# Kernel tuning notes

Hardware: AMD Instinct MI355X
Metric: run time of the kernel (lower is better)

## Reference

```python
import jax, jax.numpy as jnp
import numpy as np

B, C, H, W = 8, 4, 96, 96
HW = H * W
PCT = 95.0            # TRUNCATED_HAUSDORFF_PERCENTILE
IGNORE = 0            # HD_IGNORE_CLASS_INDEX


def setup_inputs() -> dict:
    key = jax.random.key(0)
    k1, k2 = jax.random.split(key)
    predictions = jax.random.normal(k1, (B, C, H, W), dtype=jnp.float32)
    labels = jax.random.randint(k2, (B, H, W), 0, C, dtype=jnp.int32)
    return {"predictions": predictions, "labels": labels}


def _masked_percentile(vals, mask, q):
    """np.percentile(vals[mask], q) with linear interpolation; invalid -> +inf sort to end."""
    n = jnp.sum(mask)
    s = jnp.sort(jnp.where(mask, vals, jnp.inf))
    pos = (q / 100.0) * jnp.maximum(n - 1, 0).astype(vals.dtype)
    lo = jnp.floor(pos).astype(jnp.int32)
    hi = jnp.ceil(pos).astype(jnp.int32)
    frac = pos - lo.astype(vals.dtype)
    return s[lo] * (1.0 - frac) + s[hi] * frac


def _hausdorff(predictions, labels):
    # argmax of softmax == argmax of logits, but keep the softmax for faithfulness
    pred_cls = jnp.argmax(jax.nn.softmax(predictions, axis=1), axis=1)  # [B,H,W]
    cls_ids = jnp.arange(C)
    mask_a = (pred_cls[:, None] == cls_ids[None, :, None, None]).reshape(B * C, HW)  # pred one-hot
    mask_b = (labels[:, None] == cls_ids[None, :, None, None]).reshape(B * C, HW)    # label one-hot

    # Pixel coordinates (row, col) as in np.argwhere; pairwise Euclidean distances once.
    ys, xs = jnp.meshgrid(jnp.arange(H), jnp.arange(W), indexing="ij")
    coords = jnp.stack([ys.ravel(), xs.ravel()], axis=1).astype(jnp.float32)  # [HW,2]
    sq = jnp.sum(coords * coords, axis=1)
    D = jnp.sqrt(jnp.maximum(sq[:, None] + sq[None, :] - 2.0 * (coords @ coords.T), 0.0))  # [HW,HW]

    def per_pair(masks):
        ma, mb = masks  # [HW] bool each
        fwd_min = jnp.min(jnp.where(mb[None, :], D, jnp.inf), axis=1)  # min dist A-pixel -> B set
        rev_min = jnp.min(jnp.where(ma[:, None], D, jnp.inf), axis=0)  # min dist B-pixel -> A set
        f = _masked_percentile(fwd_min, ma, PCT)
        r = _masked_percentile(rev_min, mb, PCT)
        return jnp.stack([f, r, jnp.maximum(f, r)])

    res = jax.lax.map(per_pair, (mask_a, mask_b)).reshape(B, C, 3)
    valid = (jnp.arange(C) != IGNORE)
    per_class = jnp.where(valid[None, :, None], res, 0.0).mean(axis=0)  # [C,3] mean over batch

    def finalize(v):  # v: [C] -> [C+2]: per-class, mean(all), mean(excluding class 0)
        return jnp.concatenate([v, jnp.mean(v)[None], jnp.mean(v[1:])[None]])

    FHD = finalize(per_class[:, 0])
    RHD = finalize(per_class[:, 1])
    MHD = finalize(per_class[:, 2])
    return MHD, FHD, RHD


def reference(predictions, labels):
    return _hausdorff(predictions, labels)
```

## Files before the change

kernel.cpp:

```cpp
#include <hip/hip_runtime.h>
#include <math.h>

#define B_   8
#define C_   4
#define H_   96
#define W_   96
#define HW_  9216
#define NBINS 18052
#define NH32 ((NBINS + 1) / 2)
#define NT   1024
#define NBLK 64
#define NW   16
#define NGRP 1152

__global__ __launch_bounds__(NT) void hd_main(const float* __restrict__ preds,
                                              const int*   __restrict__ labels,
                                              float* __restrict__ frws)
{
    __shared__ unsigned char  qmb[NGRP];
    __shared__ unsigned char  tmb[NGRP];
    __shared__ unsigned short g2u[HW_];
    __shared__ unsigned int   h32[NH32];
    __shared__ int twv[NW], qwv[NW], zwv[NW], bwv[NW];

    const int id  = blockIdx.x;
    const int dir = id & 1;
    const int bc  = id >> 1;
    const int b   = bc >> 2;
    const int c   = bc & 3;
    const int tid = threadIdx.x;
    const int lane = tid & 63;
    const int wid  = tid >> 6;

    const float* Pb = preds  + (size_t)b * C_ * HW_;
    const int*   Lb = labels + (size_t)b * HW_;

    for (int i = tid; i < NH32; i += NT) h32[i] = 0u;

    {
        int myT = 0, myQ = 0, myN0 = 0;
        #pragma unroll
        for (int k = 0; k < 2; ++k) {
            const int g = k * NT + tid;
            if (g < NGRP) {
                const int bp = g * 8;
                const float4 a0 = *(const float4*)(Pb + bp);
                const float4 b0 = *(const float4*)(Pb + bp + 4);
                const float4 a1 = *(const float4*)(Pb + HW_ + bp);
                const float4 b1 = *(const float4*)(Pb + HW_ + bp + 4);
                const float4 a2 = *(const float4*)(Pb + 2 * HW_ + bp);
                const float4 b2 = *(const float4*)(Pb + 2 * HW_ + bp + 4);
                const float4 a3 = *(const float4*)(Pb + 3 * HW_ + bp);
                const float4 b3 = *(const float4*)(Pb + 3 * HW_ + bp + 4);
                const int4   l0 = *(const int4*)(Lb + bp);
                const int4   l1 = *(const int4*)(Lb + bp + 4);
                unsigned tb = 0, qb = 0;
                #define PX_(j, e0, e1, e2, e3, lj)                              \
                {   int bi = 0; float bv = (e0);                                \
                    if ((e1) > bv) { bv = (e1); bi = 1; }                       \
                    if ((e2) > bv) { bv = (e2); bi = 2; }                       \
                    if ((e3) > bv) { bv = (e3); bi = 3; }                       \
                    const bool pm = (bi == c);                                  \
                    const bool lm = ((lj) == c);                                \
                    const bool qm = dir ? lm : pm;                              \
                    const bool tm = dir ? pm : lm;                              \
                    tb |= (unsigned)tm << (j); qb |= (unsigned)qm << (j); }
                PX_(0, a0.x, a1.x, a2.x, a3.x, l0.x)
                PX_(1, a0.y, a1.y, a2.y, a3.y, l0.y)
                PX_(2, a0.z, a1.z, a2.z, a3.z, l0.z)
                PX_(3, a0.w, a1.w, a2.w, a3.w, l0.w)
                PX_(4, b0.x, b1.x, b2.x, b3.x, l1.x)
                PX_(5, b0.y, b1.y, b2.y, b3.y, l1.y)
                PX_(6, b0.z, b1.z, b2.z, b3.z, l1.z)
                PX_(7, b0.w, b1.w, b2.w, b3.w, l1.w)
                #undef PX_
                tmb[g] = (unsigned char)tb;
                qmb[g] = (unsigned char)qb;
                myT  += __popc(tb);
                myQ  += __popc(qb);
                myN0 += __popc(tb & qb);
            }
        }
        #pragma unroll
        for (int d = 32; d >= 1; d >>= 1) {
            myT  += __shfl_xor(myT,  d, 64);
            myQ  += __shfl_xor(myQ,  d, 64);
            myN0 += __shfl_xor(myN0, d, 64);
        }
        if (lane == 0) { twv[wid] = myT; qwv[wid] = myQ; zwv[wid] = myN0; }
    }
    __syncthreads();

    int nT = 0;
    #pragma unroll
    for (int w = 0; w < NW; ++w) nT += twv[w];
    const int tEmpty = (nT == 0);

    for (int k = 0; k < HW_ / NT; ++k) {
        const int p = k * NT + tid;
        const int y = p / W_;
        const int x = p - y * W_;
        const unsigned r0 = *(const unsigned*)(tmb + 12 * y);
        const unsigned r1 = *(const unsigned*)(tmb + 12 * y + 4);
        const unsigned r2 = *(const unsigned*)(tmb + 12 * y + 8);
        const unsigned long long A  = (unsigned long long)r0 |
                                      ((unsigned long long)r1 << 32);
        const unsigned long long Bw = r2;

        int dl = 1000, dr = 1000;
        if (x < 64) {
            const unsigned long long ml = A & ((2ull << x) - 1ull);
            if (ml) dl = x - (63 - __builtin_clzll(ml));
            const unsigned long long mr = A & ~((1ull << x) - 1ull);
            if (mr)      dr = __builtin_ctzll(mr) - x;
            else if (Bw) dr = 64 + __builtin_ctzll(Bw) - x;
        } else {
            const int xb = x - 64;
            const unsigned long long ml = Bw & ((2ull << xb) - 1ull);
            if (ml)     dl = x - (64 + 63 - __builtin_clzll(ml));
            else if (A) dl = x - (63 - __builtin_clzll(A));
            const unsigned long long mr = Bw & ~((1ull << xb) - 1ull);
            if (mr) dr = 64 + __builtin_ctzll(mr) - x;
        }
        const int g = min(dl, dr);
        g2u[p] = (g >= 96) ? (unsigned short)40000
                           : (unsigned short)(g * g);
    }
    __syncthreads();

    {
        int bmax = 0;
        if (!tEmpty) {
            for (int k = 0; k < HW_ / NT; ++k) {
                const int p = k * NT + tid;
                const int byi = p >> 3, bsh = p & 7;
                if (!((qmb[byi] >> bsh) & 1)) continue;
                if ((tmb[byi] >> bsh) & 1) continue;
                const int y = p / W_;
                const int x = p - y * W_;
                const int a0 = (int)g2u[p];
                const int a1 = (y >= 1)     ? (int)g2u[p - W_]     : 0x7FFF0000;
                const int a2 = (y + 1 < H_) ? (int)g2u[p + W_]     : 0x7FFF0000;
                const int a3 = (y >= 2)     ? (int)g2u[p - 2 * W_] : 0x7FFF0000;
                const int a4 = (y + 2 < H_) ? (int)g2u[p + 2 * W_] : 0x7FFF0000;
                int best = min(a0, min(min(a1 + 1, a2 + 1), min(a3 + 4, a4 + 4)));
                for (int off = 3; off < H_; ++off) {
                    const int o2 = off * off;
                    if (o2 >= best) break;
                    const int r1 = y - off;
                    const int r2 = y + off;
                    if (r1 >= 0) best = min(best, o2 + (int)g2u[r1 * W_ + x]);
                    if (r2 < H_) best = min(best, o2 + (int)g2u[r2 * W_ + x]);
                }
                bmax = max(bmax, best);
                atomicAdd(&h32[best >> 1], 1u << ((best & 1) << 4));
            }
        }
        #pragma unroll
        for (int d = 32; d >= 1; d >>= 1) bmax = max(bmax, __shfl_xor(bmax, d, 64));
        if (lane == 0) bwv[wid] = bmax;
    }
    __syncthreads();

    if (wid != 0) return;

    int nQ = 0, n0s = 0, maxd2 = 0;
    #pragma unroll
    for (int w = 0; w < NW; ++w) {
        nQ += qwv[w]; n0s += zwv[w]; maxd2 = max(maxd2, bwv[w]);
    }
    const int h0x = tEmpty ? 0 : n0s;

    int nm1 = nQ - 1; if (nm1 < 0) nm1 = 0;
    const float posf = 0.95f * (float)nm1;
    const int lo = (int)floorf(posf);
    const int hi = (int)ceilf(posf);
    const float frac = posf - (float)lo;

    int svlo = -1, svhi = -1;
    if (!tEmpty) {
        int run = 0;
        for (int base = 0; base <= maxd2; base += 64) {
            const int i = base + lane;
            int h = 0;
            if (i <= maxd2) {
                h = (int)((h32[i >> 1] >> ((i & 1) << 4)) & 0xFFFFu);
                if (i == 0) h += h0x;
            }
            int inc = h;
            #pragma unroll
            for (int d = 1; d < 64; d <<= 1) {
                const int t = __shfl_up(inc, d, 64);
                if (lane >= d) inc += t;
            }
            const int excl = run + inc - h;
            if (h > 0) {
                if (excl <= lo && lo < excl + h) svlo = i;
                if (excl <= hi && hi < excl + h) svhi = i;
            }
            run += __shfl(inc, 63, 64);
        }
        #pragma unroll
        for (int d = 32; d >= 1; d >>= 1) {
            svlo = max(svlo, __shfl_xor(svlo, d, 64));
            svhi = max(svhi, __shfl_xor(svhi, d, 64));
        }
    }
    if (lane == 0) {
        const float vlo = (svlo < 0) ? __builtin_inff() : (float)sqrt((double)svlo);
        const float vhi = (svhi < 0) ? __builtin_inff() : (float)sqrt((double)svhi);
        frws[id] = vlo * (1.0f - frac) + vhi * frac;
    }
}

__global__ __launch_bounds__(64) void hd_fin(const float* __restrict__ frws,
                                             float* __restrict__ out)
{
    __shared__ float fr[NBLK];
    const int tid = threadIdx.x;
    fr[tid] = frws[tid];
    __syncthreads();
    if (tid == 0) {
        float F[4], R[4], M[4];
        for (int c = 0; c < 4; ++c) {
            if (c == 0) { F[c] = R[c] = M[c] = 0.0f; continue; }
            float sf = 0.0f, sr = 0.0f, sm = 0.0f;
            for (int b = 0; b < 8; ++b) {
                const float f = fr[((b * 4 + c) << 1) + 0];
                const float r = fr[((b * 4 + c) << 1) + 1];
                sf += f; sr += r;
                float m = f > r ? f : r;
                if (f != f || r != r) m = f + r;
                sm += m;
            }
            F[c] = sf / 8.0f; R[c] = sr / 8.0f; M[c] = sm / 8.0f;
        }
        float* o = out;
        o[0] = M[0]; o[1] = M[1]; o[2] = M[2]; o[3] = M[3];
        o[4] = (M[0] + M[1] + M[2] + M[3]) / 4.0f;
        o[5] = (M[1] + M[2] + M[3]) / 3.0f;
        o += 6;
        o[0] = F[0]; o[1] = F[1]; o[2] = F[2]; o[3] = F[3];
        o[4] = (F[0] + F[1] + F[2] + F[3]) / 4.0f;
        o[5] = (F[1] + F[2] + F[3]) / 3.0f;
        o += 6;
        o[0] = R[0]; o[1] = R[1]; o[2] = R[2]; o[3] = R[3];
        o[4] = (R[0] + R[1] + R[2] + R[3]) / 4.0f;
        o[5] = (R[1] + R[2] + R[3]) / 3.0f;
    }
}

extern "C" void kernel_launch(void* const* d_in, const int* in_sizes, int n_in,
                              void* d_out, int out_size, void* d_ws, size_t ws_size,
                              hipStream_t stream)
{
    const float* preds  = (const float*)d_in[0];
    const int*   labels = (const int*)d_in[1];
    float* frws = (float*)d_ws;

    hipLaunchKernelGGL(hd_main, dim3(NBLK), dim3(NT), 0, stream,
                       preds, labels, frws);
    hipLaunchKernelGGL(hd_fin, dim3(1), dim3(64), 0, stream,
                       frws, (float*)d_out);
}
```

Baseline: 20.40 us.

## Skip ignored class blocks, add per-warp low-bin histograms, parallelize finalize

The main grid shrinks from 64 to 48 blocks by never launching the class-0 blocks, since their result is zeroed anyway. Small squared distances below 128 now go into per-warp privatized shared histograms, which cuts atomic contention on hot bins. The prefix scan sums these per-warp copies for the low bins. The finalize kernel computes its 18 outputs in parallel across threads instead of on a single thread; the class-0 slots in the workspace are left unwritten but are not read.

```diff
diff --git a/kernel.cpp b/kernel.cpp
--- a/kernel.cpp
+++ b/kernel.cpp
@@ -9,9 +9,10 @@
 #define NBINS 18052
 #define NH32 ((NBINS + 1) / 2)
 #define NT   1024
-#define NBLK 64
 #define NW   16
 #define NGRP 1152
+#define NBLK 48
+#define HOT  128
 
 __global__ __launch_bounds__(NT) void hd_main(const float* __restrict__ preds,
                                               const int*   __restrict__ labels,
@@ -21,13 +22,15 @@
     __shared__ unsigned char  tmb[NGRP];
     __shared__ unsigned short g2u[HW_];
     __shared__ unsigned int   h32[NH32];
+    __shared__ unsigned int   whist[NW * (HOT / 2)];
     __shared__ int twv[NW], qwv[NW], zwv[NW], bwv[NW];
 
-    const int id  = blockIdx.x;
-    const int dir = id & 1;
-    const int bc  = id >> 1;
-    const int b   = bc >> 2;
-    const int c   = bc & 3;
+    const int bid = blockIdx.x;
+    const int b   = bid / 6;
+    const int rem = bid - b * 6;
+    const int c   = 1 + (rem >> 1);
+    const int dir = rem & 1;
+    const int id  = ((b * 4 + c) << 1) | dir;
     const int tid = threadIdx.x;
     const int lane = tid & 63;
     const int wid  = tid >> 6;
@@ -36,7 +39,7 @@
     const int*   Lb = labels + (size_t)b * HW_;
 
     for (int i = tid; i < NH32; i += NT) h32[i] = 0u;
-
+    whist[tid >> 0] = 0u;
     {
         int myT = 0, myQ = 0, myN0 = 0;
         #pragma unroll
@@ -130,6 +133,7 @@
 
     {
         int bmax = 0;
+        unsigned int* wh = whist + wid * (HOT / 2);
         if (!tEmpty) {
             for (int k = 0; k < HW_ / NT; ++k) {
                 const int p = k * NT + tid;
@@ -153,7 +157,9 @@
                     if (r2 < H_) best = min(best, o2 + (int)g2u[r2 * W_ + x]);
                 }
                 bmax = max(bmax, best);
-                atomicAdd(&h32[best >> 1], 1u << ((best & 1) << 4));
+                const unsigned inc = 1u << ((best & 1) << 4);
+                if (best < HOT) atomicAdd(&wh[best >> 1], inc);
+                else            atomicAdd(&h32[best >> 1], inc);
             }
         }
         #pragma unroll
@@ -184,8 +190,16 @@
             const int i = base + lane;
             int h = 0;
             if (i <= maxd2) {
-                h = (int)((h32[i >> 1] >> ((i & 1) << 4)) & 0xFFFFu);
-                if (i == 0) h += h0x;
+                if (i == 0) {
+                    h = h0x;
+                } else if (i < HOT) {
+                    const int wofs = i >> 1, hsh = (i & 1) << 4;
+                    #pragma unroll
+                    for (int w = 0; w < NW; ++w)
+                        h += (int)((whist[w * (HOT / 2) + wofs] >> hsh) & 0xFFFFu);
+                } else {
+                    h = (int)((h32[i >> 1] >> ((i & 1) << 4)) & 0xFFFFu);
+                }
             }
             int inc = h;
             #pragma unroll
@@ -216,38 +230,40 @@
 __global__ __launch_bounds__(64) void hd_fin(const float* __restrict__ frws,
                                              float* __restrict__ out)
 {
-    __shared__ float fr[NBLK];
+    __shared__ float fr[64];
     const int tid = threadIdx.x;
     fr[tid] = frws[tid];
     __syncthreads();
-    if (tid == 0) {
-        float F[4], R[4], M[4];
-        for (int c = 0; c < 4; ++c) {
-            if (c == 0) { F[c] = R[c] = M[c] = 0.0f; continue; }
-            float sf = 0.0f, sr = 0.0f, sm = 0.0f;
-            for (int b = 0; b < 8; ++b) {
-                const float f = fr[((b * 4 + c) << 1) + 0];
-                const float r = fr[((b * 4 + c) << 1) + 1];
-                sf += f; sr += r;
-                float m = f > r ? f : r;
-                if (f != f || r != r) m = f + r;
-                sm += m;
-            }
-            F[c] = sf / 8.0f; R[c] = sr / 8.0f; M[c] = sm / 8.0f;
-        }
-        float* o = out;
-        o[0] = M[0]; o[1] = M[1]; o[2] = M[2]; o[3] = M[3];
-        o[4] = (M[0] + M[1] + M[2] + M[3]) / 4.0f;
-        o[5] = (M[1] + M[2] + M[3]) / 3.0f;
-        o += 6;
-        o[0] = F[0]; o[1] = F[1]; o[2] = F[2]; o[3] = F[3];
-        o[4] = (F[0] + F[1] + F[2] + F[3]) / 4.0f;
-        o[5] = (F[1] + F[2] + F[3]) / 3.0f;
-        o += 6;
-        o[0] = R[0]; o[1] = R[1]; o[2] = R[2]; o[3] = R[3];
-        o[4] = (R[0] + R[1] + R[2] + R[3]) / 4.0f;
-        o[5] = (R[1] + R[2] + R[3]) / 3.0f;
-    }
+    if (tid >= 18) return;
+    const int sec = tid / 6;
+    const int j   = tid - sec * 6;
+
+    auto classval = [&](int c) -> float {
+        float s = 0.0f;
+        for (int b = 0; b < 8; ++b) {
+            const float f = fr[((b * 4 + c) << 1) + 0];
+            const float r = fr[((b * 4 + c) << 1) + 1];
+            float v;
+            if (sec == 1)      v = f;
+            else if (sec == 2) v = r;
+            else {
+                v = f > r ? f : r;
+                if (f != f || r != r) v = f + r;
+            }
+            s += v;
+        }
+        return s / 8.0f;
+    };
+
+    float res;
+    if (j < 4) {
+        res = (j == 0) ? 0.0f : classval(j);
+    } else {
+        const float v1 = classval(1), v2 = classval(2), v3 = classval(3);
+        if (j == 4) res = (0.0f + v1 + v2 + v3) / 4.0f;
+        else        res = (v1 + v2 + v3) / 3.0f;
+    }
+    out[sec * 6 + j] = res;
 }
 
 extern "C" void kernel_launch(void* const* d_in, const int* in_sizes, int n_in,
```

After: 22.00 us. 7.8% more time.
